# Kernel optimization log

Hardware: AMD Instinct MI355X
Metric: run time of the kernel (lower is better)

The kernel has to match this reference:

```python
import jax, jax.numpy as jnp
import numpy as np

B, T, H, NH, EL = 64, 1024, 256, 4, 768
DH = H // NH
EPS = 1e-3


def _ln(x, g, b):
    mu = jnp.mean(x, axis=-1, keepdims=True)
    var = jnp.var(x, axis=-1, keepdims=True)
    return (x - mu) * jax.lax.rsqrt(var + EPS) * g + b


def _glu(x, W, b):
    y = x @ W.T + b
    a, gate = jnp.split(y, 2, axis=-1)
    return a * jax.nn.sigmoid(gate)


def setup_inputs() -> dict:
    key = jax.random.key(0)
    ks = iter(jax.random.split(key, 40))
    w = lambda *s: jax.random.normal(next(ks), s, jnp.float32) * 0.02
    inp = {
        "temporal_features": jax.random.normal(next(ks), (B, T, H), jnp.float32),
        "ce": jax.random.normal(next(ks), (B, H), jnp.float32),
        # enrichment GRN (with context)
        "eg_Wa": w(H, H), "eg_ba": jnp.zeros((H,), jnp.float32),
        "eg_Wc": w(H, H),
        "eg_Wi": w(H, H), "eg_bi": jnp.zeros((H,), jnp.float32),
        "eg_Wg": w(2 * H, H), "eg_bg": jnp.zeros((2 * H,), jnp.float32),
        "eg_lng": jnp.ones((H,), jnp.float32), "eg_lnb": jnp.zeros((H,), jnp.float32),
        # interpretable MHA
        "att_Wqkv": w((2 * NH + 1) * DH, H),
        "att_Wout": w(H, DH),
        # attention gate + LN
        "ag_W": w(2 * H, H), "ag_b": jnp.zeros((2 * H,), jnp.float32),
        "aln_g": jnp.ones((H,), jnp.float32), "aln_b": jnp.zeros((H,), jnp.float32),
        # positionwise GRN (no context)
        "pg_Wa": w(H, H), "pg_ba": jnp.zeros((H,), jnp.float32),
        "pg_Wi": w(H, H), "pg_bi": jnp.zeros((H,), jnp.float32),
        "pg_Wg": w(2 * H, H), "pg_bg": jnp.zeros((2 * H,), jnp.float32),
        "pg_lng": jnp.ones((H,), jnp.float32), "pg_lnb": jnp.zeros((H,), jnp.float32),
        # decoder gate + LN
        "dg_W": w(2 * H, H), "dg_b": jnp.zeros((2 * H,), jnp.float32),
        "dln_g": jnp.ones((H,), jnp.float32), "dln_b": jnp.zeros((H,), jnp.float32),
    }
    return inp


def _forward(temporal_features, ce,
             eg_Wa, eg_ba, eg_Wc, eg_Wi, eg_bi, eg_Wg, eg_bg, eg_lng, eg_lnb,
             att_Wqkv, att_Wout,
             ag_W, ag_b, aln_g, aln_b,
             pg_Wa, pg_ba, pg_Wi, pg_bi, pg_Wg, pg_bg, pg_lng, pg_lnb,
             dg_W, dg_b, dln_g, dln_b):
    # enrichment GRN: linear + context -> ELU -> linear -> GLU -> residual -> LN
    x = temporal_features @ eg_Wa.T + eg_ba + (ce @ eg_Wc.T)[:, None, :]
    x = jax.nn.elu(x)
    x = x @ eg_Wi.T + eg_bi
    x = _glu(x, eg_Wg, eg_bg)
    enriched = _ln(x + temporal_features, eg_lng, eg_lnb)

    # interpretable multi-head attention (shared V, head-averaged output)
    qkv = enriched @ att_Wqkv.T  # [B,T,(2*NH+1)*DH]
    q = qkv[..., : NH * DH].reshape(B, T, NH, DH)
    k = qkv[..., NH * DH: 2 * NH * DH].reshape(B, T, NH, DH)
    v = qkv[..., 2 * NH * DH:]  # [B,T,DH]
    scale = DH ** -0.5
    scores = jnp.einsum("bthd,bshd->bhts", q, k) * scale  # [B,NH,T,T]
    mask = jnp.triu(jnp.full((T, T), -jnp.inf, jnp.float32), k=1)
    probs = jax.nn.softmax(scores + mask, axis=-1)
    attn_vec = jnp.einsum("bhts,bsd->bhtd", probs, v)  # [B,NH,T,DH]
    m_attn = jnp.mean(attn_vec, axis=1)  # [B,T,DH]
    a = m_attn @ att_Wout.T  # [B,T,H]

    # slice to decoder steps
    a = a[:, EL:, :]
    tf_dec = temporal_features[:, EL:, :]
    enr_dec = enriched[:, EL:, :]

    x = _glu(a, ag_W, ag_b)
    x = _ln(x + enr_dec, aln_g, aln_b)

    # positionwise GRN
    y = jax.nn.elu(x @ pg_Wa.T + pg_ba)
    y = y @ pg_Wi.T + pg_bi
    y = _glu(y, pg_Wg, pg_bg)
    x = _ln(y + x, pg_lng, pg_lnb)

    x = _glu(x, dg_W, dg_b)
    x = _ln(x + tf_dec, dln_g, dln_b)
    return x


def reference(temporal_features, ce,
              eg_Wa, eg_ba, eg_Wc, eg_Wi, eg_bi, eg_Wg, eg_bg, eg_lng, eg_lnb,
              att_Wqkv, att_Wout,
              ag_W, ag_b, aln_g, aln_b,
              pg_Wa, pg_ba, pg_Wi, pg_bi, pg_Wg, pg_bg, pg_lng, pg_lnb,
              dg_W, dg_b, dln_g, dln_b):
    return _forward(temporal_features, ce,
                    eg_Wa, eg_ba, eg_Wc, eg_Wi, eg_bi, eg_Wg, eg_bg, eg_lng, eg_lnb,
                    att_Wqkv, att_Wout,
                    ag_W, ag_b, aln_g, aln_b,
                    pg_Wa, pg_ba, pg_Wi, pg_bi, pg_Wg, pg_bg, pg_lng, pg_lnb,
                    dg_W, dg_b, dln_g, dln_b)
```

## Files before the change

### kernel.cpp

```cpp
#include <hip/hip_runtime.h>
#include <hip/hip_bf16.h>
#include <math.h>

typedef __hip_bfloat16 bf16;
typedef unsigned short u16;
typedef unsigned int u32;
typedef __attribute__((ext_vector_type(8))) short bfrag8;
typedef __attribute__((ext_vector_type(8))) _Float16 hfrag8;
typedef __attribute__((ext_vector_type(4))) float f32x4;

constexpr int Bb = 64, Tt = 1024, Hh = 256, NHn = 4, DHd = 64, ELe = 768;
constexpr int TD = Tt - ELe;
constexpr int BT = Bb * Tt;
constexpr int BD = Bb * TD;
constexpr float QSCALE = 0.18033688011112042f;

__device__ __forceinline__ bool probe_bf16(const void* probe) {
    return *(const unsigned int*)probe == 0x3F803F80u;
}
__device__ __forceinline__ float bfbits2f(unsigned short u) {
    union { unsigned int i; float f; } c; c.i = ((unsigned int)u) << 16; return c.f;
}
__device__ __forceinline__ u16 f2bf(float f) {
    union { float f; unsigned int u; } c; c.f = f;
    unsigned int r = c.u + 0x7fffu + ((c.u >> 16) & 1u);
    return (u16)(r >> 16);
}
__device__ __forceinline__ u16 f2h(float f) {
    union { _Float16 h; u16 u; } c; c.h = (_Float16)f; return c.u;
}
__device__ __forceinline__ float h2f(u16 u) {
    union { u16 u; _Float16 h; } c; c.u = u; return (float)c.h;
}
__device__ __forceinline__ float4 load4dt(const void* p, long idx, bool bf) {
    if (bf) {
        ushort4 u = *(const ushort4*)((const unsigned short*)p + idx);
        return make_float4(bfbits2f(u.x), bfbits2f(u.y), bfbits2f(u.z), bfbits2f(u.w));
    }
    return *(const float4*)((const float*)p + idx);
}
__device__ __forceinline__ float load1dt(const void* p, long idx, bool bf) {
    return bf ? bfbits2f(((const unsigned short*)p)[idx]) : ((const float*)p)[idx];
}
__device__ __forceinline__ int swz(int row, int k) {
    return row * 64 + ((((k >> 3) ^ (row & 7)) << 3) | (k & 7));
}
__device__ __forceinline__ void gload16(const void* g, void* l) {
    __builtin_amdgcn_global_load_lds(
        (const __attribute__((address_space(1))) void*)g,
        (__attribute__((address_space(3))) void*)l, 16, 0, 0);
}
__device__ __forceinline__ u32 cvtpk(float a, float b) {
    u32 r; asm("v_cvt_pk_bf16_f32 %0, %1, %2" : "=v"(r) : "v"(a), "v"(b)); return r;
}

__global__ __launch_bounds__(256) void cvt_f16(const void* __restrict__ src,
                                               u16* __restrict__ dst,
                                               long n4, const void* __restrict__ probe)
{
    const bool dtb = probe_bf16(probe);
    long i = (long)blockIdx.x * 256 + threadIdx.x;
    long stride = (long)gridDim.x * 256;
    for (; i < n4; i += stride) {
        float4 v = load4dt(src, i * 4, dtb);
        ushort4 o = make_ushort4(f2h(v.x), f2h(v.y), f2h(v.z), f2h(v.w));
        *(ushort4*)&dst[i * 4] = o;
    }
}

__global__ __launch_bounds__(256) void cvtw_all(
    const void* s0, const void* s1, const void* s2, const void* s3,
    const void* s4, const void* s5, const void* s6, const void* s7,
    const void* s8, const void* s9, u16* __restrict__ dst,
    const void* __restrict__ probe)
{
    const bool dtb = probe_bf16(probe);
    int blk = blockIdx.x;
    const void* src; long seg0, base;
    if      (blk < 64)  { src = s0; seg0 = 0;   base = 0;      }
    else if (blk < 128) { src = s1; seg0 = 64;  base = 65536;  }
    else if (blk < 256) { src = s2; seg0 = 128; base = 131072; }
    else if (blk < 400) { src = s3; seg0 = 256; base = 262144; }
    else if (blk < 416) { src = s4; seg0 = 400; base = 409600; }
    else if (blk < 544) { src = s5; seg0 = 416; base = 425984; }
    else if (blk < 608) { src = s6; seg0 = 544; base = 557056; }
    else if (blk < 672) { src = s7; seg0 = 608; base = 622592; }
    else if (blk < 800) { src = s8; seg0 = 672; base = 688128; }
    else                { src = s9; seg0 = 800; base = 819200; }
    long i = (long)(blk - seg0) * 1024 + (long)threadIdx.x * 4;
    float4 v = load4dt(src, i, dtb);
    ushort4 o = make_ushort4(f2h(v.x), f2h(v.y), f2h(v.z), f2h(v.w));
    *(ushort4*)&dst[base + i] = o;
}

__global__ __launch_bounds__(256) void ceproj_kernel(const void* __restrict__ ce,
                                                     const void* __restrict__ Wc,
                                                     const void* __restrict__ probe,
                                                     float* __restrict__ out)
{
    const bool bf = probe_bf16(probe);
    __shared__ float ces[256];
    int b = blockIdx.x, tid = threadIdx.x;
    ces[tid] = load1dt(ce, b * 256 + tid, bf);
    __syncthreads();
    float acc = 0.f;
    #pragma unroll 4
    for (int k = 0; k < 256; k += 4) {
        float4 w4 = load4dt(Wc, (long)tid * 256 + k, bf);
        acc = fmaf(ces[k], w4.x, acc);
        acc = fmaf(ces[k + 1], w4.y, acc);
        acc = fmaf(ces[k + 2], w4.z, acc);
        acc = fmaf(ces[k + 3], w4.w, acc);
    }
    out[b * 256 + tid] = acc;
}

__global__ __launch_bounds__(256, 2) void gemm_mfma(
    const u16* __restrict__ A_g, const u16* __restrict__ W_g,
    const void* __restrict__ bias,
    const float* __restrict__ ceproj,
    const void* __restrict__ res0,
    void* __restrict__ Cout,
    const void* __restrict__ probe,
    int M, int N, int K, int mode,
    int res_kind, int a_decmap, int res_decmap, int out_kind)
{
    const int tid = threadIdx.x;
    const int w = tid >> 6, lane = tid & 63, lr = lane & 15, lg = lane >> 4;
    const int wm = w >> 1, wn = w & 1;
    const int m0 = blockIdx.x * 128;
    const int n0 = blockIdx.y * 128;
    const int n0g = blockIdx.y * 64;

    __shared__ __align__(16) u16 AsF[2][128 * 64];
    __shared__ __align__(16) u16 WsF[2][128 * 64];

    const int sl8 = lane >> 3;
    const int slot = lane & 7;

    long aoff[4]; long woff[4];
    #pragma unroll
    for (int i = 0; i < 4; ++i) {
        int row = w * 32 + i * 8 + sl8;
        int gm = m0 + row;
        long ar = a_decmap ? ((long)(gm >> 8) * 1024 + 768 + (gm & 255)) : (long)gm;
        aoff[i] = ar * K + (long)((slot ^ (row & 7)) * 8);
        int wr;
        if (mode == 3) {
            int g = row >> 5;
            wr = ((g & 1) ? 256 : 0) + n0g + ((g >> 1) << 5) + (row & 31);
        } else {
            wr = n0 + row; if (wr > N - 1) wr = N - 1;
        }
        woff[i] = (long)wr * K + (long)((slot ^ (row & 7)) * 8);
    }

    f32x4 acc[4][4];
    #pragma unroll
    for (int i = 0; i < 4; ++i)
        #pragma unroll
        for (int j = 0; j < 4; ++j) acc[i][j] = (f32x4){0.f, 0.f, 0.f, 0.f};

    #pragma unroll
    for (int i = 0; i < 4; ++i) {
        int rbase = w * 32 + i * 8;
        gload16(A_g + aoff[i], &AsF[0][rbase * 64]);
        gload16(W_g + woff[i], &WsF[0][rbase * 64]);
    }

    int cur = 0;
    for (int kt = 0; kt < K; kt += 64) {
        __syncthreads();
        if (kt + 64 < K) {
            #pragma unroll
            for (int i = 0; i < 4; ++i) {
                int rbase = w * 32 + i * 8;
                gload16(A_g + aoff[i] + kt + 64, &AsF[cur ^ 1][rbase * 64]);
                gload16(W_g + woff[i] + kt + 64, &WsF[cur ^ 1][rbase * 64]);
            }
        }
        #pragma unroll
        for (int kh = 0; kh < 2; ++kh) {
            hfrag8 wf[4];
            #pragma unroll
            for (int j = 0; j < 4; ++j)
                wf[j] = *(const hfrag8*)&WsF[cur][swz(wn * 64 + j * 16 + lr, kh * 32 + lg * 8)];
            #pragma unroll
            for (int i = 0; i < 4; ++i) {
                hfrag8 ah = *(const hfrag8*)&AsF[cur][swz(wm * 64 + i * 16 + lr, kh * 32 + lg * 8)];
                #pragma unroll
                for (int j = 0; j < 4; ++j)
                    acc[i][j] = __builtin_amdgcn_mfma_f32_16x16x32_f16(ah, wf[j], acc[i][j], 0, 0, 0);
            }
        }
        cur ^= 1;
    }

    const bool dtb = probe_bf16(probe);
    #pragma unroll
    for (int i = 0; i < 4; ++i) {
        #pragma unroll
        for (int r = 0; r < 4; ++r) {
            int gm = m0 + wm * 64 + i * 16 + lg * 4 + r;
            if (mode == 3) {
                long rrow = res_decmap ? ((long)(gm >> 8) * 1024 + 768 + (gm & 255)) : (long)gm;
                #pragma unroll
                for (int jj = 0; jj < 2; ++jj) {
                    int c = n0g + wn * 32 + jj * 16 + lr;
                    float a = acc[i][jj][r]     + load1dt(bias, c, dtb);
                    float g = acc[i][jj + 2][r] + load1dt(bias, c + 256, dtb);
                    float rv;
                    if (res_kind == 1) rv = h2f(((const u16*)res0)[rrow * 256 + c]);
                    else               rv = load1dt(res0, rrow * 256 + c, dtb);
                    float o = a / (1.f + __expf(-g)) + rv;
                    long ci = (long)gm * 256 + c;
                    if (out_kind == 2) ((u16*)Cout)[ci] = f2h(o);
                    else               ((float*)Cout)[ci] = o;
                }
            } else {
                #pragma unroll
                for (int j = 0; j < 4; ++j) {
                    int n = n0 + wn * 64 + j * 16 + lr;
                    if (n < N) {
                        float v = acc[i][j][r];
                        if (bias) v += load1dt(bias, n, dtb);
                        if (mode == 1) v += ceproj[((gm >> 10) << 8) + n];
                        if (mode >= 1) v = (v > 0.f) ? v : (__expf(v) - 1.f);
                        long ci = (long)gm * N + n;
                        if (out_kind == 0)      ((float*)Cout)[ci] = v;
                        else if (out_kind == 1) ((u16*)Cout)[ci] = f2bf(v);
                        else if (out_kind == 3) ((u16*)Cout)[ci] = f2bf(v * QSCALE);
                        else                    ((u16*)Cout)[ci] = f2h(v);
                    }
                }
            }
        }
    }
}

__global__ __launch_bounds__(256) void ln_kernel(const u16* __restrict__ vin,
                                                 const void* __restrict__ g,
                                                 const void* __restrict__ beta,
                                                 void* __restrict__ out,
                                                 const void* __restrict__ probe,
                                                 int out_kind)
{
    const bool dtb = probe_bf16(probe);
    int tid = threadIdx.x;
    long m = (long)blockIdx.x * 4 + (tid >> 6);
    int l = tid & 63;
    ushort4 raw = *(const ushort4*)&vin[m * 256 + l * 4];
    float v0 = h2f(raw.x), v1 = h2f(raw.y), v2 = h2f(raw.z), v3 = h2f(raw.w);
    float s  = v0 + v1 + v2 + v3;
    float s2 = v0 * v0 + v1 * v1 + v2 * v2 + v3 * v3;
    #pragma unroll
    for (int off = 32; off > 0; off >>= 1) {
        s  += __shfl_xor(s, off);
        s2 += __shfl_xor(s2, off);
    }
    float mu  = s * (1.f / 256.f);
    float var = s2 * (1.f / 256.f) - mu * mu;
    float rstd = rsqrtf(var + 1e-3f);
    float4 gg = load4dt(g, l * 4, dtb);
    float4 bb = load4dt(beta, l * 4, dtb);
    float y0 = (v0 - mu) * rstd * gg.x + bb.x;
    float y1 = (v1 - mu) * rstd * gg.y + bb.y;
    float y2 = (v2 - mu) * rstd * gg.z + bb.z;
    float y3 = (v3 - mu) * rstd * gg.w + bb.w;
    long idx = m * 256 + l * 4;
    if (out_kind == 2) {
        *(ushort4*)&((u16*)out)[idx] = make_ushort4(f2h(y0), f2h(y1), f2h(y2), f2h(y3));
    } else if (dtb) {
        *(ushort4*)&((u16*)out)[idx] = make_ushort4(f2bf(y0), f2bf(y1), f2bf(y2), f2bf(y3));
    } else {
        *(float4*)&((float*)out)[idx] = make_float4(y0, y1, y2, y3);
    }
}

__global__ __launch_bounds__(256) void vtrans(const u16* __restrict__ vtmp,
                                              u16* __restrict__ vt)
{
    int b  = blockIdx.x >> 4;
    int s0 = (blockIdx.x & 15) << 6;
    __shared__ u16 t[64][72];
    int tid = threadIdx.x;
    {
        int sl = tid >> 4;
        int d0 = (tid & 15) << 2;
        #pragma unroll
        for (int u = 0; u < 4; ++u) {
            int s = u * 16 + sl;
            ushort4 v4 = *(const ushort4*)&vtmp[((long)(b * 1024 + s0 + s)) * 64 + d0];
            t[d0 + 0][s] = v4.x; t[d0 + 1][s] = v4.y;
            t[d0 + 2][s] = v4.z; t[d0 + 3][s] = v4.w;
        }
    }
    __syncthreads();
    {
        int d = tid >> 2, c0 = (tid & 3) << 4;
        u16* dst = vt + ((long)(b * 64 + d)) * 1024 + s0 + c0;
        *(uint4*)dst       = *(const uint4*)&t[d][c0];
        *(uint4*)(dst + 8) = *(const uint4*)&t[d][c0 + 8];
    }
}

__global__ __launch_bounds__(256) void attn_mfma(const u16* __restrict__ qd,
                                                 const u16* __restrict__ kb,
                                                 const u16* __restrict__ vt,
                                                 float* __restrict__ Oscr)
{
    int bid = blockIdx.x;
    int qt = bid & 3, h = (bid >> 2) & 3, b = bid >> 4;
    int tid = threadIdx.x;
    int w = tid >> 6, lane = tid & 63, lr = lane & 15, lg = lane >> 4;
    const int sl8 = lane >> 3, slot = lane & 7;

    __shared__ __align__(16) u16 Ks[2][64 * 64];
    __shared__ __align__(16) u16 Vs[2][64 * 64];

    bfrag8 qf0, qf1;
    {
        long tok = (long)b * 256 + qt * 64 + w * 16 + lr;
        const u16* qp = qd + tok * 256 + h * 64 + lg * 8;
        qf0 = *(const bfrag8*)(qp);
        qf1 = *(const bfrag8*)(qp + 32);
    }

    f32x4 O[4];
    float m_i = -INFINITY, l_i = 0.f;
    #pragma unroll
    for (int jd = 0; jd < 4; ++jd) O[jd] = (f32x4){0.f, 0.f, 0.f, 0.f};
    const int qabs = 768 + qt * 64 + w * 16 + lr;

    const int srcA = lr + ((lg & 1) ? 32 : 0);
    const int srcB = srcA + 16;
    const bool hi = (lg >= 2);
    const int ntiles = 13 + qt;

    const long kbase = (long)b * 1024 * 256 + h * 64;
    const long vbase = (long)b * 64 * 1024;

    #pragma unroll
    for (int i = 0; i < 2; ++i) {
        int rbase = w * 16 + i * 8;
        int row = rbase + sl8;
        int sw = (slot ^ (row & 7)) * 8;
        gload16(kb + kbase + (long)row * 256 + sw, &Ks[0][rbase * 64]);
        gload16(vt + vbase + (long)row * 1024 + sw, &Vs[0][rbase * 64]);
    }

    int cur = 0;
    for (int st = 0; st < ntiles; ++st) {
        int s0 = st * 64;
        __syncthreads();
        if (st + 1 < ntiles) {
            int s1 = s0 + 64;
            #pragma unroll
            for (int i = 0; i < 2; ++i) {
                int rbase = w * 16 + i * 8;
                int row = rbase + sl8;
                int sw = (slot ^ (row & 7)) * 8;
                gload16(kb + kbase + (long)(s1 + row) * 256 + sw, &Ks[cur ^ 1][rbase * 64]);
                gload16(vt + vbase + (long)row * 1024 + s1 + sw, &Vs[cur ^ 1][rbase * 64]);
            }
        }

        f32x4 sv[4];
        #pragma unroll
        for (int jb = 0; jb < 4; ++jb) {
            f32x4 a = (f32x4){0.f, 0.f, 0.f, 0.f};
            a = __builtin_amdgcn_mfma_f32_16x16x32_bf16(
                    *(const bfrag8*)&Ks[cur][swz(jb * 16 + lr, lg * 8)], qf0, a, 0, 0, 0);
            a = __builtin_amdgcn_mfma_f32_16x16x32_bf16(
                    *(const bfrag8*)&Ks[cur][swz(jb * 16 + lr, 32 + lg * 8)], qf1, a, 0, 0, 0);
            sv[jb] = a;
        }

        if (st == ntiles - 1) {
            #pragma unroll
            for (int jb = 0; jb < 4; ++jb)
                #pragma unroll
                for (int r = 0; r < 4; ++r)
                    if (s0 + jb * 16 + lg * 4 + r > qabs) sv[jb][r] = -INFINITY;
        }

        float mx = -INFINITY;
        #pragma unroll
        for (int jb = 0; jb < 4; ++jb)
            #pragma unroll
            for (int r = 0; r < 4; ++r) mx = fmaxf(mx, sv[jb][r]);
        mx = fmaxf(mx, __shfl_xor(mx, 16));
        mx = fmaxf(mx, __shfl_xor(mx, 32));
        float mnew = fmaxf(m_i, mx);
        float alpha = exp2f(m_i - mnew);
        float ps = 0.f;
        #pragma unroll
        for (int jb = 0; jb < 4; ++jb)
            #pragma unroll
            for (int r = 0; r < 4; ++r) {
                float p = exp2f(sv[jb][r] - mnew);
                sv[jb][r] = p; ps += p;
            }
        ps += __shfl_xor(ps, 16);
        ps += __shfl_xor(ps, 32);
        l_i = l_i * alpha + ps;
        m_i = mnew;

        float alr[4];
        #pragma unroll
        for (int r = 0; r < 4; ++r) alr[r] = __shfl(alpha, lg * 4 + r);
        #pragma unroll
        for (int jd = 0; jd < 4; ++jd)
            #pragma unroll
            for (int r = 0; r < 4; ++r) O[jd][r] *= alr[r];

        u32 c0_[2], c1_[2], c2_[2], c3_[2];
        c0_[0] = cvtpk(sv[0][0], sv[0][1]); c0_[1] = cvtpk(sv[0][2], sv[0][3]);
        c1_[0] = cvtpk(sv[1][0], sv[1][1]); c1_[1] = cvtpk(sv[1][2], sv[1][3]);
        c2_[0] = cvtpk(sv[2][0], sv[2][1]); c2_[1] = cvtpk(sv[2][2], sv[2][3]);
        c3_[0] = cvtpk(sv[3][0], sv[3][1]); c3_[1] = cvtpk(sv[3][2], sv[3][3]);

        #pragma unroll
        for (int sh = 0; sh < 2; ++sh) {
            u32 lo0 = sh ? c2_[0] : c0_[0], lo1 = sh ? c2_[1] : c0_[1];
            u32 hi0 = sh ? c3_[0] : c1_[0], hi1 = sh ? c3_[1] : c1_[1];
            u32 a0 = (u32)__shfl((int)lo0, srcA), a1 = (u32)__shfl((int)lo1, srcA);
            u32 A0 = (u32)__shfl((int)hi0, srcA), A1 = (u32)__shfl((int)hi1, srcA);
            u32 b0 = (u32)__shfl((int)lo0, srcB), b1 = (u32)__shfl((int)lo1, srcB);
            u32 B0 = (u32)__shfl((int)hi0, srcB), B1 = (u32)__shfl((int)hi1, srcB);
            union { u32 u[4]; bfrag8 v; } pu;
            pu.u[0] = hi ? A0 : a0; pu.u[1] = hi ? A1 : a1;
            pu.u[2] = hi ? B0 : b0; pu.u[3] = hi ? B1 : b1;
            #pragma unroll
            for (int jd = 0; jd < 4; ++jd) {
                bfrag8 vb = *(const bfrag8*)&Vs[cur][swz(jd * 16 + lr, sh * 32 + lg * 8)];
                O[jd] = __builtin_amdgcn_mfma_f32_16x16x32_bf16(pu.v, vb, O[jd], 0, 0, 0);
            }
        }
        cur ^= 1;
    }

    float inv = 1.f / l_i;
    float linv[4];
    #pragma unroll
    for (int r = 0; r < 4; ++r) linv[r] = __shfl(inv, lg * 4 + r);
    #pragma unroll
    for (int jd = 0; jd < 4; ++jd)
        #pragma unroll
        for (int r = 0; r < 4; ++r) {
            long token = (long)b * 256 + qt * 64 + w * 16 + lg * 4 + r;
            Oscr[token * 256 + h * 64 + jd * 16 + lr] = O[jd][r] * linv[r];
        }
}

__global__ __launch_bounds__(256) void headmean(const float* __restrict__ O,
                                                u16* __restrict__ outH)
{
    int i = blockIdx.x * 256 + threadIdx.x;
    int token = i >> 6, d = i & 63;
    const float* p = O + (long)token * 256 + d;
    float m = 0.25f * (p[0] + p[64] + p[128] + p[192]);
    outH[i] = f2h(m);
}

extern "C" void kernel_launch(void* const* d_in, const int* in_sizes, int n_in,
                              void* d_out, int out_size, void* d_ws, size_t ws_size,
                              hipStream_t stream)
{
    const void* tf       = d_in[0];
    const void* ce       = d_in[1];
    const void* eg_Wa    = d_in[2];
    const void* eg_ba    = d_in[3];
    const void* eg_Wc    = d_in[4];
    const void* eg_Wi    = d_in[5];
    const void* eg_bi    = d_in[6];
    const void* eg_Wg    = d_in[7];
    const void* eg_bg    = d_in[8];
    const void* eg_lng   = d_in[9];
    const void* eg_lnb   = d_in[10];
    const void* att_Wqkv = d_in[11];
    const void* att_Wout = d_in[12];
    const void* ag_W     = d_in[13];
    const void* ag_b     = d_in[14];
    const void* aln_g    = d_in[15];
    const void* aln_b    = d_in[16];
    const void* pg_Wa    = d_in[17];
    const void* pg_ba    = d_in[18];
    const void* pg_Wi    = d_in[19];
    const void* pg_bi    = d_in[20];
    const void* pg_Wg    = d_in[21];
    const void* pg_bg    = d_in[22];
    const void* pg_lng   = d_in[23];
    const void* pg_lnb   = d_in[24];
    const void* dg_W     = d_in[25];
    const void* dg_b     = d_in[26];
    const void* dln_g    = d_in[27];
    const void* dln_b    = d_in[28];
    const void* probe    = eg_lng;

    float* ws = (float*)d_ws;

    const long CEP = 0;
    const long WPo = 65536;
    const long P   = 1114112;
    const long Q   = P + 8388608L;
    const long T   = Q + 16777216L;

    float* ceprojF = ws + CEP;

    u16* wp = (u16*)(ws + WPo);
    u16* WaH = wp + 0;      u16* WiH = wp + 65536;  u16* WgH = wp + 131072;
    u16* WqH = wp + 262144; u16* WoH = wp + 409600; u16* AgH = wp + 425984;
    u16* PaH = wp + 557056; u16* PiH = wp + 622592; u16* PgH = wp + 688128;
    u16* DgH = wp + 819200;

    u16* tfH   = (u16*)(ws + P);
    u16* g1H   = (u16*)(ws + Q);
    u16* x2H   = (u16*)(ws + Q + 8388608L);
    u16* glu3H = (u16*)(ws + Q);
    u16* enrH  = (u16*)(ws + T);

    u16*   kvbK = (u16*)(ws + Q);
    u16*   vtmp = (u16*)(ws + Q + 8388608L);
    u16*   qd16 = (u16*)(ws + Q + 8388608L + 2097152L);
    u16*   vt16 = (u16*)(ws + Q + 8388608L + 4194304L);
    float* Oscr = ws + P;
    u16*   matnH = (u16*)(ws + P + 4194304L);

    u16* D[8];
    for (int k = 0; k < 8; ++k) D[k] = (u16*)(ws + Q + (long)k * 2097152L);

    dim3 blk(256);
    auto cgrid = [](long n4) {
        long g = (n4 + 255) / 256; if (g > 2048) g = 2048; return dim3((unsigned)g);
    };
    const long NBT = (long)BT * 256;

    cvt_f16<<<cgrid(NBT / 4), blk, 0, stream>>>(tf, tfH, NBT / 4, probe);
    cvtw_all<<<928, blk, 0, stream>>>(eg_Wa, eg_Wi, eg_Wg, att_Wqkv, att_Wout,
                                      ag_W, pg_Wa, pg_Wi, pg_Wg, dg_W, wp, probe);
    ceproj_kernel<<<64, blk, 0, stream>>>(ce, eg_Wc, probe, ceprojF);

    gemm_mfma<<<dim3(BT / 128, 2), blk, 0, stream>>>(
        tfH, WaH, eg_ba, ceprojF, nullptr, g1H, probe, BT, 256, 256, 1, 0, 0, 0, 2);
    gemm_mfma<<<dim3(BT / 128, 2), blk, 0, stream>>>(
        g1H, WiH, eg_bi, nullptr, nullptr, x2H, probe, BT, 256, 256, 0, 0, 0, 0, 2);
    gemm_mfma<<<dim3(BT / 128, 4), blk, 0, stream>>>(
        x2H, WgH, eg_bg, nullptr, tf, glu3H, probe, BT, 256, 256, 3, 0, 0, 0, 2);
    ln_kernel<<<BT / 4, blk, 0, stream>>>(glu3H, eg_lng, eg_lnb, enrH, probe, 2);

    gemm_mfma<<<dim3(BT / 128, 2), blk, 0, stream>>>(
        enrH, WqH + (long)256 * 256, nullptr, nullptr, nullptr, kvbK, probe,
        BT, 256, 256, 0, 0, 0, 0, 1);
    gemm_mfma<<<dim3(BT / 128, 1), blk, 0, stream>>>(
        enrH, WqH + (long)512 * 256, nullptr, nullptr, nullptr, vtmp, probe,
        BT, 64, 256, 0, 0, 0, 0, 1);
    gemm_mfma<<<dim3(BD / 128, 2), blk, 0, stream>>>(
        enrH, WqH, nullptr, nullptr, nullptr, qd16, probe,
        BD, 256, 256, 0, 0, 1, 0, 3);
    vtrans<<<1024, blk, 0, stream>>>(vtmp, vt16);

    attn_mfma<<<Bb * NHn * 4, blk, 0, stream>>>(qd16, kvbK, vt16, Oscr);
    headmean<<<(BD * 64) / 256, blk, 0, stream>>>(Oscr, matnH);

    gemm_mfma<<<dim3(BD / 128, 2), blk, 0, stream>>>(
        matnH, WoH, nullptr, nullptr, nullptr, D[0], probe, BD, 256, 64, 0, 0, 0, 0, 2);
    gemm_mfma<<<dim3(BD / 128, 4), blk, 0, stream>>>(
        D[0], AgH, ag_b, nullptr, enrH, D[1], probe, BD, 256, 256, 3, 1, 0, 1, 2);
    ln_kernel<<<BD / 4, blk, 0, stream>>>(D[1], aln_g, aln_b, D[2], probe, 2);
    gemm_mfma<<<dim3(BD / 128, 2), blk, 0, stream>>>(
        D[2], PaH, pg_ba, nullptr, nullptr, D[3], probe, BD, 256, 256, 2, 0, 0, 0, 2);
    gemm_mfma<<<dim3(BD / 128, 2), blk, 0, stream>>>(
        D[3], PiH, pg_bi, nullptr, nullptr, D[4], probe, BD, 256, 256, 0, 0, 0, 0, 2);
    gemm_mfma<<<dim3(BD / 128, 4), blk, 0, stream>>>(
        D[4], PgH, pg_bg, nullptr, D[2], D[5], probe, BD, 256, 256, 3, 1, 0, 0, 2);
    ln_kernel<<<BD / 4, blk, 0, stream>>>(D[5], pg_lng, pg_lnb, D[6], probe, 2);
    gemm_mfma<<<dim3(BD / 128, 4), blk, 0, stream>>>(
        D[6], DgH, dg_b, nullptr, tf, D[7], probe, BD, 256, 256, 3, 0, 0, 1, 2);
    ln_kernel<<<BD / 4, blk, 0, stream>>>(D[7], dln_g, dln_b, d_out, probe, 1);
}
```

Baseline: 655.9 us.

## Merge K and V projections into one GEMM and single-buffer GEMM LDS

Measured after the change: 593.6 us. -9.5%, faster.

```diff
diff --git a/kernel.cpp b/kernel.cpp
--- a/kernel.cpp
+++ b/kernel.cpp
@@ -13,6 +13,7 @@
 constexpr int TD = Tt - ELe;
 constexpr int BT = Bb * Tt;
 constexpr int BD = Bb * TD;
+constexpr int KVS = 320;
 constexpr float QSCALE = 0.18033688011112042f;
 
 __device__ __forceinline__ bool probe_bf16(const void* probe) {
@@ -115,7 +116,7 @@
     out[b * 256 + tid] = acc;
 }
 
-__global__ __launch_bounds__(256, 2) void gemm_mfma(
+__global__ __launch_bounds__(256, 4) void gemm_mfma(
     const u16* __restrict__ A_g, const u16* __restrict__ W_g,
     const void* __restrict__ bias,
     const float* __restrict__ ceproj,
@@ -132,8 +133,8 @@
     const int n0 = blockIdx.y * 128;
     const int n0g = blockIdx.y * 64;
 
-    __shared__ __align__(16) u16 AsF[2][128 * 64];
-    __shared__ __align__(16) u16 WsF[2][128 * 64];
+    __shared__ __align__(16) u16 AsF[128 * 64];
+    __shared__ __align__(16) u16 WsF[128 * 64];
 
     const int sl8 = lane >> 3;
     const int slot = lane & 7;
@@ -161,39 +162,30 @@
         #pragma unroll
         for (int j = 0; j < 4; ++j) acc[i][j] = (f32x4){0.f, 0.f, 0.f, 0.f};
 
-    #pragma unroll
-    for (int i = 0; i < 4; ++i) {
-        int rbase = w * 32 + i * 8;
-        gload16(A_g + aoff[i], &AsF[0][rbase * 64]);
-        gload16(W_g + woff[i], &WsF[0][rbase * 64]);
-    }
-
-    int cur = 0;
     for (int kt = 0; kt < K; kt += 64) {
         __syncthreads();
-        if (kt + 64 < K) {
-            #pragma unroll
-            for (int i = 0; i < 4; ++i) {
-                int rbase = w * 32 + i * 8;
-                gload16(A_g + aoff[i] + kt + 64, &AsF[cur ^ 1][rbase * 64]);
-                gload16(W_g + woff[i] + kt + 64, &WsF[cur ^ 1][rbase * 64]);
-            }
-        }
+        #pragma unroll
+        for (int i = 0; i < 4; ++i) {
+            int rbase = w * 32 + i * 8;
+            gload16(A_g + aoff[i] + kt, &AsF[rbase * 64]);
+            gload16(W_g + woff[i] + kt, &WsF[rbase * 64]);
+        }
+        __syncthreads();
+
         #pragma unroll
         for (int kh = 0; kh < 2; ++kh) {
             hfrag8 wf[4];
             #pragma unroll
             for (int j = 0; j < 4; ++j)
-                wf[j] = *(const hfrag8*)&WsF[cur][swz(wn * 64 + j * 16 + lr, kh * 32 + lg * 8)];
+                wf[j] = *(const hfrag8*)&WsF[swz(wn * 64 + j * 16 + lr, kh * 32 + lg * 8)];
             #pragma unroll
             for (int i = 0; i < 4; ++i) {
-                hfrag8 ah = *(const hfrag8*)&AsF[cur][swz(wm * 64 + i * 16 + lr, kh * 32 + lg * 8)];
+                hfrag8 ah = *(const hfrag8*)&AsF[swz(wm * 64 + i * 16 + lr, kh * 32 + lg * 8)];
                 #pragma unroll
                 for (int j = 0; j < 4; ++j)
                     acc[i][j] = __builtin_amdgcn_mfma_f32_16x16x32_f16(ah, wf[j], acc[i][j], 0, 0, 0);
             }
         }
-        cur ^= 1;
     }
 
     const bool dtb = probe_bf16(probe);
@@ -277,7 +269,7 @@
     }
 }
 
-__global__ __launch_bounds__(256) void vtrans(const u16* __restrict__ vtmp,
+__global__ __launch_bounds__(256) void vtrans(const u16* __restrict__ kvb,
                                               u16* __restrict__ vt)
 {
     int b  = blockIdx.x >> 4;
@@ -290,7 +282,7 @@
         #pragma unroll
         for (int u = 0; u < 4; ++u) {
             int s = u * 16 + sl;
-            ushort4 v4 = *(const ushort4*)&vtmp[((long)(b * 1024 + s0 + s)) * 64 + d0];
+            ushort4 v4 = *(const ushort4*)&kvb[((long)(b * 1024 + s0 + s)) * KVS + 256 + d0];
             t[d0 + 0][s] = v4.x; t[d0 + 1][s] = v4.y;
             t[d0 + 2][s] = v4.z; t[d0 + 3][s] = v4.w;
         }
@@ -337,7 +329,7 @@
     const bool hi = (lg >= 2);
     const int ntiles = 13 + qt;
 
-    const long kbase = (long)b * 1024 * 256 + h * 64;
+    const long kbase = (long)b * 1024 * KVS + h * 64;
     const long vbase = (long)b * 64 * 1024;
 
     #pragma unroll
@@ -345,7 +337,7 @@
         int rbase = w * 16 + i * 8;
         int row = rbase + sl8;
         int sw = (slot ^ (row & 7)) * 8;
-        gload16(kb + kbase + (long)row * 256 + sw, &Ks[0][rbase * 64]);
+        gload16(kb + kbase + (long)row * KVS + sw, &Ks[0][rbase * 64]);
         gload16(vt + vbase + (long)row * 1024 + sw, &Vs[0][rbase * 64]);
     }
 
@@ -360,7 +352,7 @@
                 int rbase = w * 16 + i * 8;
                 int row = rbase + sl8;
                 int sw = (slot ^ (row & 7)) * 8;
-                gload16(kb + kbase + (long)(s1 + row) * 256 + sw, &Ks[cur ^ 1][rbase * 64]);
+                gload16(kb + kbase + (long)(s1 + row) * KVS + sw, &Ks[cur ^ 1][rbase * 64]);
                 gload16(vt + vbase + (long)row * 1024 + s1 + sw, &Vs[cur ^ 1][rbase * 64]);
             }
         }
@@ -520,10 +512,9 @@
     u16* glu3H = (u16*)(ws + Q);
     u16* enrH  = (u16*)(ws + T);
 
-    u16*   kvbK = (u16*)(ws + Q);
-    u16*   vtmp = (u16*)(ws + Q + 8388608L);
-    u16*   qd16 = (u16*)(ws + Q + 8388608L + 2097152L);
-    u16*   vt16 = (u16*)(ws + Q + 8388608L + 4194304L);
+    u16*   kvb  = (u16*)(ws + Q);
+    u16*   qd16 = (u16*)(ws + Q + 10485760L);
+    u16*   vt16 = (u16*)(ws + Q + 12582912L);
     float* Oscr = ws + P;
     u16*   matnH = (u16*)(ws + P + 4194304L);
 
@@ -549,18 +540,15 @@
         x2H, WgH, eg_bg, nullptr, tf, glu3H, probe, BT, 256, 256, 3, 0, 0, 0, 2);
     ln_kernel<<<BT / 4, blk, 0, stream>>>(glu3H, eg_lng, eg_lnb, enrH, probe, 2);
 
-    gemm_mfma<<<dim3(BT / 128, 2), blk, 0, stream>>>(
-        enrH, WqH + (long)256 * 256, nullptr, nullptr, nullptr, kvbK, probe,
-        BT, 256, 256, 0, 0, 0, 0, 1);
-    gemm_mfma<<<dim3(BT / 128, 1), blk, 0, stream>>>(
-        enrH, WqH + (long)512 * 256, nullptr, nullptr, nullptr, vtmp, probe,
-        BT, 64, 256, 0, 0, 0, 0, 1);
+    gemm_mfma<<<dim3(BT / 128, 3), blk, 0, stream>>>(
+        enrH, WqH + (long)256 * 256, nullptr, nullptr, nullptr, kvb, probe,
+        BT, 320, 256, 0, 0, 0, 0, 1);
     gemm_mfma<<<dim3(BD / 128, 2), blk, 0, stream>>>(
         enrH, WqH, nullptr, nullptr, nullptr, qd16, probe,
         BD, 256, 256, 0, 0, 1, 0, 3);
-    vtrans<<<1024, blk, 0, stream>>>(vtmp, vt16);
-
-    attn_mfma<<<Bb * NHn * 4, blk, 0, stream>>>(qd16, kvbK, vt16, Oscr);
+    vtrans<<<1024, blk, 0, stream>>>(kvb, vt16);
+
+    attn_mfma<<<Bb * NHn * 4, blk, 0, stream>>>(qd16, kvb, vt16, Oscr);
     headmean<<<(BD * 64) / 256, blk, 0, stream>>>(Oscr, matnH);
 
     gemm_mfma<<<dim3(BD / 128, 2), blk, 0, stream>>>(
```

## Single-buffer GEMM LDS, raise occupancy, add 64-row tile GEMM for decoder

Applied to the files above, without the earlier changes.

Measured after the change: 553.6 us. 15.6% less time.

```diff
diff --git a/kernel.cpp b/kernel.cpp
--- a/kernel.cpp
+++ b/kernel.cpp
@@ -115,7 +115,8 @@
     out[b * 256 + tid] = acc;
 }
 
-__global__ __launch_bounds__(256, 2) void gemm_mfma(
+
+__global__ __launch_bounds__(256, 3) void gemm_mfma(
     const u16* __restrict__ A_g, const u16* __restrict__ W_g,
     const void* __restrict__ bias,
     const float* __restrict__ ceproj,
@@ -125,6 +126,7 @@
     int M, int N, int K, int mode,
     int res_kind, int a_decmap, int res_decmap, int out_kind)
 {
+    const bool dtb = probe_bf16(probe);
     const int tid = threadIdx.x;
     const int w = tid >> 6, lane = tid & 63, lr = lane & 15, lg = lane >> 4;
     const int wm = w >> 1, wn = w & 1;
@@ -132,8 +134,8 @@
     const int n0 = blockIdx.y * 128;
     const int n0g = blockIdx.y * 64;
 
-    __shared__ __align__(16) u16 AsF[2][128 * 64];
-    __shared__ __align__(16) u16 WsF[2][128 * 64];
+    __shared__ __align__(16) u16 AsF[128 * 64];
+    __shared__ __align__(16) u16 WsF[128 * 64];
 
     const int sl8 = lane >> 3;
     const int slot = lane & 7;
@@ -161,42 +163,32 @@
         #pragma unroll
         for (int j = 0; j < 4; ++j) acc[i][j] = (f32x4){0.f, 0.f, 0.f, 0.f};
 
-    #pragma unroll
-    for (int i = 0; i < 4; ++i) {
-        int rbase = w * 32 + i * 8;
-        gload16(A_g + aoff[i], &AsF[0][rbase * 64]);
-        gload16(W_g + woff[i], &WsF[0][rbase * 64]);
-    }
-
-    int cur = 0;
     for (int kt = 0; kt < K; kt += 64) {
         __syncthreads();
-        if (kt + 64 < K) {
-            #pragma unroll
-            for (int i = 0; i < 4; ++i) {
-                int rbase = w * 32 + i * 8;
-                gload16(A_g + aoff[i] + kt + 64, &AsF[cur ^ 1][rbase * 64]);
-                gload16(W_g + woff[i] + kt + 64, &WsF[cur ^ 1][rbase * 64]);
-            }
-        }
+        #pragma unroll
+        for (int i = 0; i < 4; ++i) {
+            int rbase = w * 32 + i * 8;
+            gload16(A_g + aoff[i] + kt, &AsF[rbase * 64]);
+            gload16(W_g + woff[i] + kt, &WsF[rbase * 64]);
+        }
+        __syncthreads();
+
         #pragma unroll
         for (int kh = 0; kh < 2; ++kh) {
             hfrag8 wf[4];
             #pragma unroll
             for (int j = 0; j < 4; ++j)
-                wf[j] = *(const hfrag8*)&WsF[cur][swz(wn * 64 + j * 16 + lr, kh * 32 + lg * 8)];
+                wf[j] = *(const hfrag8*)&WsF[swz(wn * 64 + j * 16 + lr, kh * 32 + lg * 8)];
             #pragma unroll
             for (int i = 0; i < 4; ++i) {
-                hfrag8 ah = *(const hfrag8*)&AsF[cur][swz(wm * 64 + i * 16 + lr, kh * 32 + lg * 8)];
+                hfrag8 ah = *(const hfrag8*)&AsF[swz(wm * 64 + i * 16 + lr, kh * 32 + lg * 8)];
                 #pragma unroll
                 for (int j = 0; j < 4; ++j)
                     acc[i][j] = __builtin_amdgcn_mfma_f32_16x16x32_f16(ah, wf[j], acc[i][j], 0, 0, 0);
             }
         }
-        cur ^= 1;
-    }
-
-    const bool dtb = probe_bf16(probe);
+    }
+
     #pragma unroll
     for (int i = 0; i < 4; ++i) {
         #pragma unroll
@@ -238,6 +230,123 @@
     }
 }
 
+__global__ __launch_bounds__(256, 4) void gemm_mfma64(
+    const u16* __restrict__ A_g, const u16* __restrict__ W_g,
+    const void* __restrict__ bias,
+    const float* __restrict__ ceproj,
+    const void* __restrict__ res0,
+    void* __restrict__ Cout,
+    const void* __restrict__ probe,
+    int M, int N, int K, int mode,
+    int res_kind, int a_decmap, int res_decmap, int out_kind)
+{
+    const bool dtb = probe_bf16(probe);
+    const int tid = threadIdx.x;
+    const int w = tid >> 6, lane = tid & 63, lr = lane & 15, lg = lane >> 4;
+    const int wm = w >> 1, wn = w & 1;
+    const int m0 = blockIdx.x * 64;
+    const int n0 = blockIdx.y * 128;
+    const int n0g = blockIdx.y * 64;
+
+    __shared__ __align__(16) u16 AsF[64 * 64];
+    __shared__ __align__(16) u16 WsF[128 * 64];
+
+    const int sl8 = lane >> 3, slot = lane & 7;
+
+    long aoff[2]; long woff[4];
+    #pragma unroll
+    for (int i = 0; i < 2; ++i) {
+        int row = i * 32 + w * 8 + sl8;
+        int gm = m0 + row;
+        long ar = a_decmap ? ((long)(gm >> 8) * 1024 + 768 + (gm & 255)) : (long)gm;
+        aoff[i] = ar * K + (long)((slot ^ (row & 7)) * 8);
+    }
+    #pragma unroll
+    for (int i = 0; i < 4; ++i) {
+        int row = i * 32 + w * 8 + sl8;
+        int wr;
+        if (mode == 3) {
+            int g = row >> 5;
+            wr = ((g & 1) ? 256 : 0) + n0g + ((g >> 1) << 5) + (row & 31);
+        } else {
+            wr = n0 + row; if (wr > N - 1) wr = N - 1;
+        }
+        woff[i] = (long)wr * K + (long)((slot ^ (row & 7)) * 8);
+    }
+
+    f32x4 acc[2][4];
+    #pragma unroll
+    for (int i = 0; i < 2; ++i)
+        #pragma unroll
+        for (int j = 0; j < 4; ++j) acc[i][j] = (f32x4){0.f, 0.f, 0.f, 0.f};
+
+    for (int kt = 0; kt < K; kt += 64) {
+        __syncthreads();
+        #pragma unroll
+        for (int i = 0; i < 2; ++i)
+            gload16(A_g + aoff[i] + kt, &AsF[(i * 32 + w * 8) * 64]);
+        #pragma unroll
+        for (int i = 0; i < 4; ++i)
+            gload16(W_g + woff[i] + kt, &WsF[(i * 32 + w * 8) * 64]);
+        __syncthreads();
+
+        #pragma unroll
+        for (int kh = 0; kh < 2; ++kh) {
+            hfrag8 wf[4];
+            #pragma unroll
+            for (int j = 0; j < 4; ++j)
+                wf[j] = *(const hfrag8*)&WsF[swz(wn * 64 + j * 16 + lr, kh * 32 + lg * 8)];
+            #pragma unroll
+            for (int i = 0; i < 2; ++i) {
+                hfrag8 ah = *(const hfrag8*)&AsF[swz(wm * 32 + i * 16 + lr, kh * 32 + lg * 8)];
+                #pragma unroll
+                for (int j = 0; j < 4; ++j)
+                    acc[i][j] = __builtin_amdgcn_mfma_f32_16x16x32_f16(ah, wf[j], acc[i][j], 0, 0, 0);
+            }
+        }
+    }
+
+    #pragma unroll
+    for (int i = 0; i < 2; ++i) {
+        #pragma unroll
+        for (int r = 0; r < 4; ++r) {
+            int gm = m0 + wm * 32 + i * 16 + lg * 4 + r;
+            if (mode == 3) {
+                long rrow = res_decmap ? ((long)(gm >> 8) * 1024 + 768 + (gm & 255)) : (long)gm;
+                #pragma unroll
+                for (int jj = 0; jj < 2; ++jj) {
+                    int c = n0g + wn * 32 + jj * 16 + lr;
+                    float a = acc[i][jj][r]     + load1dt(bias, c, dtb);
+                    float g = acc[i][jj + 2][r] + load1dt(bias, c + 256, dtb);
+                    float rv;
+                    if (res_kind == 1) rv = h2f(((const u16*)res0)[rrow * 256 + c]);
+                    else               rv = load1dt(res0, rrow * 256 + c, dtb);
+                    float o = a / (1.f + __expf(-g)) + rv;
+                    long ci = (long)gm * 256 + c;
+                    if (out_kind == 2) ((u16*)Cout)[ci] = f2h(o);
+                    else               ((float*)Cout)[ci] = o;
+                }
+            } else {
+                #pragma unroll
+                for (int j = 0; j < 4; ++j) {
+                    int n = n0 + wn * 64 + j * 16 + lr;
+                    if (n < N) {
+                        float v = acc[i][j][r];
+                        if (bias) v += load1dt(bias, n, dtb);
+                        if (mode == 1) v += ceproj[((gm >> 10) << 8) + n];
+                        if (mode >= 1) v = (v > 0.f) ? v : (__expf(v) - 1.f);
+                        long ci = (long)gm * N + n;
+                        if (out_kind == 0)      ((float*)Cout)[ci] = v;
+                        else if (out_kind == 1) ((u16*)Cout)[ci] = f2bf(v);
+                        else if (out_kind == 3) ((u16*)Cout)[ci] = f2bf(v * QSCALE);
+                        else                    ((u16*)Cout)[ci] = f2h(v);
+                    }
+                }
+            }
+        }
+    }
+}
+
 __global__ __launch_bounds__(256) void ln_kernel(const u16* __restrict__ vin,
                                                  const void* __restrict__ g,
                                                  const void* __restrict__ beta,
@@ -514,7 +623,7 @@
     u16* PaH = wp + 557056; u16* PiH = wp + 622592; u16* PgH = wp + 688128;
     u16* DgH = wp + 819200;
 
-    u16* tfH   = (u16*)(ws + P);
+    u16* tfH   = (u16*)(ws + T);
     u16* g1H   = (u16*)(ws + Q);
     u16* x2H   = (u16*)(ws + Q + 8388608L);
     u16* glu3H = (u16*)(ws + Q);
@@ -522,8 +631,8 @@
 
     u16*   kvbK = (u16*)(ws + Q);
     u16*   vtmp = (u16*)(ws + Q + 8388608L);
-    u16*   qd16 = (u16*)(ws + Q + 8388608L + 2097152L);
-    u16*   vt16 = (u16*)(ws + Q + 8388608L + 4194304L);
+    u16*   qd16 = (u16*)(ws + Q + 10485760L);
+    u16*   vt16 = (u16*)(ws + Q + 12582912L);
     float* Oscr = ws + P;
     u16*   matnH = (u16*)(ws + P + 4194304L);
 
@@ -555,7 +664,7 @@
     gemm_mfma<<<dim3(BT / 128, 1), blk, 0, stream>>>(
         enrH, WqH + (long)512 * 256, nullptr, nullptr, nullptr, vtmp, probe,
         BT, 64, 256, 0, 0, 0, 0, 1);
-    gemm_mfma<<<dim3(BD / 128, 2), blk, 0, stream>>>(
+    gemm_mfma64<<<dim3(BD / 64, 2), blk, 0, stream>>>(
         enrH, WqH, nullptr, nullptr, nullptr, qd16, probe,
         BD, 256, 256, 0, 0, 1, 0, 3);
     vtrans<<<1024, blk, 0, stream>>>(vtmp, vt16);
@@ -563,19 +672,19 @@
     attn_mfma<<<Bb * NHn * 4, blk, 0, stream>>>(qd16, kvbK, vt16, Oscr);
     headmean<<<(BD * 64) / 256, blk, 0, stream>>>(Oscr, matnH);
 
-    gemm_mfma<<<dim3(BD / 128, 2), blk, 0, stream>>>(
+    gemm_mfma64<<<dim3(BD / 64, 2), blk, 0, stream>>>(
         matnH, WoH, nullptr, nullptr, nullptr, D[0], probe, BD, 256, 64, 0, 0, 0, 0, 2);
-    gemm_mfma<<<dim3(BD / 128, 4), blk, 0, stream>>>(
+    gemm_mfma64<<<dim3(BD / 64, 4), blk, 0, stream>>>(
         D[0], AgH, ag_b, nullptr, enrH, D[1], probe, BD, 256, 256, 3, 1, 0, 1, 2);
     ln_kernel<<<BD / 4, blk, 0, stream>>>(D[1], aln_g, aln_b, D[2], probe, 2);
-    gemm_mfma<<<dim3(BD / 128, 2), blk, 0, stream>>>(
+    gemm_mfma64<<<dim3(BD / 64, 2), blk, 0, stream>>>(
         D[2], PaH, pg_ba, nullptr, nullptr, D[3], probe, BD, 256, 256, 2, 0, 0, 0, 2);
-    gemm_mfma<<<dim3(BD / 128, 2), blk, 0, stream>>>(
+    gemm_mfma64<<<dim3(BD / 64, 2), blk, 0, stream>>>(
         D[3], PiH, pg_bi, nullptr, nullptr, D[4], probe, BD, 256, 256, 0, 0, 0, 0, 2);
-    gemm_mfma<<<dim3(BD / 128, 4), blk, 0, stream>>>(
+    gemm_mfma64<<<dim3(BD / 64, 4), blk, 0, stream>>>(
         D[4], PgH, pg_bg, nullptr, D[2], D[5], probe, BD, 256, 256, 3, 1, 0, 0, 2);
     ln_kernel<<<BD / 4, blk, 0, stream>>>(D[5], pg_lng, pg_lnb, D[6], probe, 2);
-    gemm_mfma<<<dim3(BD / 128, 4), blk, 0, stream>>>(
+    gemm_mfma64<<<dim3(BD / 64, 4), blk, 0, stream>>>(
         D[6], DgH, dg_b, nullptr, tf, D[7], probe, BD, 256, 256, 3, 0, 0, 1, 2);
     ln_kernel<<<BD / 4, blk, 0, stream>>>(D[7], dln_g, dln_b, d_out, probe, 1);
 }
```
